# Performance work log

Measured on AMD Instinct MI355X. Metric: run time of the kernel, lower is better.

## Reference

```python
import jax, jax.numpy as jnp
import numpy as np

DILATIONS = (1, 2, 4, 8)
K = 3  # kernel_size
B, H, W, C = 16, 128, 128, 64
HID = 256
OUT = 64  # == C, so residual path is taken


def _depthwise(x, w, dilation):
    # x: [B,H,W,C], w: [K,K,1,C] (HWIO depthwise kernel)
    pad = dilation * (K // 2)
    return jax.lax.conv_general_dilated(
        x, w,
        window_strides=(1, 1),
        padding=[(pad, pad), (pad, pad)],
        rhs_dilation=(dilation, dilation),
        dimension_numbers=('NHWC', 'HWIO', 'NHWC'),
        feature_group_count=C,
    )


def setup_inputs() -> dict:
    key = jax.random.key(0)
    k_x, k_cw, k_w1, k_b1, k_w2, k_b2 = jax.random.split(key, 6)
    in_feat = C * (1 + len(DILATIONS))  # 320
    x = jax.random.normal(k_x, (B, H, W, C), jnp.float32)
    # depthwise kernels, one [K,K,1,C] per dilation, stacked
    conv_w = jax.random.normal(k_cw, (len(DILATIONS), K, K, 1, C), jnp.float32) * (1.0 / np.sqrt(K * K).astype(np.float32))
    W1 = jax.random.normal(k_w1, (in_feat, HID), jnp.float32) * np.float32(1.0 / np.sqrt(in_feat))
    b1 = jax.random.normal(k_b1, (HID,), jnp.float32) * 0.01
    W2 = jax.random.normal(k_w2, (HID, OUT), jnp.float32) * np.float32(1.0 / np.sqrt(HID))
    b2 = jax.random.normal(k_b2, (OUT,), jnp.float32) * 0.01
    return {"x": x, "conv_w": conv_w, "W1": W1, "b1": b1, "W2": W2, "b2": b2}


def reference(x, conv_w, W1, b1, W2, b2):
    # 1) Perception: multiscale depthwise dilated convs (same-padding per dilation)
    perceptions = [_depthwise(x, conv_w[i], d) for i, d in enumerate(DILATIONS)]
    upd_in = jnp.concatenate([x] + perceptions, axis=-1)  # [B,H,W,5C]
    # 2) Update MLP: Linear -> Dropout(eval: identity) -> GELU(exact erf) -> Linear
    h = jax.nn.gelu(upd_in @ W1 + b1, approximate=False)  # [B,H,W,HID]
    delta = h @ W2 + b2  # [B,H,W,OUT]
    # 3) out_channels == channels and (eval mode or fire_rate==1.0): plain residual
    return x + delta
```

## Files before the change

### kernel.cpp

```cpp
#include <hip/hip_runtime.h>
#include <hip/hip_fp16.h>
#include <cstdint>

#define B_   16
#define H_   128
#define W_   128
#define C_   64
#define HID_ 256
#define XELEMS (B_ * H_ * W_ * C_)

typedef _Float16 __attribute__((ext_vector_type(2))) half2v;
typedef _Float16 __attribute__((ext_vector_type(8))) half8v;
typedef __attribute__((ext_vector_type(4))) float f32x4;
typedef unsigned short ushort_t;

#define W1S_OFF 0
#define W2S_OFF 81920
#define CWH_OFF 98304
#define XH_OFF  100608
#define FEAT_OFF (XH_OFF + XELEMS)
#define FEAT_HALVES (4096ull * 16384ull)
#define WS_NEED_FULL (2ull * (FEAT_OFF + FEAT_HALVES))

__device__ __forceinline__ int hs(int row, int col) {
  return row * 256 + (((col >> 3) ^ (row & 7)) << 3) + (col & 7);
}

__device__ __forceinline__ float fast_gelu(float h) {
  float u = h * fmaf(h * h, 0.10293921f, 2.30211813f);
  float e = exp2f(-u);
  return h * __builtin_amdgcn_rcpf(1.0f + e);
}

__device__ __forceinline__ uint32_t fast_gelu_pk(float h0, float h1) {
  half2v h = __builtin_bit_cast(half2v, __builtin_amdgcn_cvt_pkrtz(h0, h1));
  const half2v c1 = {(_Float16)0.10293921f, (_Float16)0.10293921f};
  const half2v c0 = {(_Float16)2.30211813f, (_Float16)2.30211813f};
  half2v u = h * (c0 + h * h * c1);
  __half2 e = h2exp2(__hneg2(__builtin_bit_cast(__half2, u)));
  const __half2 one = __half2{(__half)1.0f, (__half)1.0f};
  __half2 s = h2rcp(__hadd2(one, e));
  __half2 g = __hmul2(__builtin_bit_cast(__half2, h), s);
  return __builtin_bit_cast(uint32_t, g);
}

__device__ __forceinline__ void stage16(const _Float16* g, ushort_t* l) {
  __builtin_amdgcn_global_load_lds(
      (const __attribute__((address_space(1))) void*)g,
      (__attribute__((address_space(3))) void*)l, 16, 0, 0);
}

__global__ void prep_kernel(const float* __restrict__ x,
                            const float* __restrict__ W1,
                            const float* __restrict__ W2,
                            const float* __restrict__ cw,
                            _Float16* __restrict__ wsb) {
  if (blockIdx.x < 393) {
    int t = blockIdx.x * 256 + threadIdx.x;
    if (t < 81920) {
      int j = t & 7, lane = (t >> 3) & 63, n16 = (t >> 9) & 15, ks = t >> 13;
      int k = ks * 32 + (lane >> 4) * 8 + j;
      int n = n16 * 16 + (lane & 15);
      wsb[W1S_OFF + t] = (_Float16)W1[k * 256 + n];
    } else if (t < 98304) {
      int t2 = t - 81920;
      int j = t2 & 7, lane = (t2 >> 3) & 63, n16 = (t2 >> 9) & 3, ks = t2 >> 11;
      int k = ks * 32 + (lane >> 4) * 8 + j;
      int n = n16 * 16 + (lane & 15);
      wsb[W2S_OFF + t2] = (_Float16)W2[k * 64 + n];
    } else if (t < 98304 + 2304) {
      int t3 = t - 98304;
      wsb[CWH_OFF + t3] = (_Float16)cw[t3];
    }
  } else {
    int i = ((blockIdx.x - 393) * 256 + threadIdx.x) * 8;
    const float4 a = *(const float4*)&x[i];
    const float4 b = *(const float4*)&x[i + 4];
    half8v o = {(_Float16)a.x, (_Float16)a.y, (_Float16)a.z, (_Float16)a.w,
                (_Float16)b.x, (_Float16)b.y, (_Float16)b.z, (_Float16)b.w};
    *(half8v*)&wsb[XH_OFF + i] = o;
  }
}

__global__ void conv_feat_kernel(const _Float16* __restrict__ xh,
                                 const _Float16* __restrict__ cwh,
                                 _Float16* __restrict__ feat) {
  const int tid   = threadIdx.x;
  const int tileX = blockIdx.x * 8;
  const int tileY = blockIdx.y * 8;
  const int batch = blockIdx.z >> 2;
  const int dd    = blockIdx.z & 3;
  const int dil   = 1 << dd;

  const _Float16* xhb = xh + (size_t)batch * (H_ * W_ * C_);
  _Float16* ft =
      feat + ((size_t)((batch * 16 + blockIdx.y) * 16 + blockIdx.x)) * 16384;

  const int quad = tid & 15;
  const int p0   = tid >> 4;
  const int ksq  = quad >> 3;
  const int c32  = (quad & 7) * 4;

  half2v w01[9], w23[9];
#pragma unroll
  for (int t = 0; t < 9; ++t) {
    uint2 wr = *(const uint2*)&cwh[(dd * 9 + t) * C_ + quad * 4];
    w01[t] = __builtin_bit_cast(half2v, wr.x);
    w23[t] = __builtin_bit_cast(half2v, wr.y);
  }

  uint2 v[4][9];
  const bool interior = (tileX >= 8) && (tileX <= W_ - 16) &&
                        (tileY >= 8) && (tileY <= H_ - 16);
  if (interior) {
#pragma unroll
    for (int i = 0; i < 4; ++i) {
      const int p  = i * 16 + p0;
      const int y0 = tileY + (p >> 3), x0 = tileX + (p & 7);
#pragma unroll
      for (int ky = 0; ky < 3; ++ky)
#pragma unroll
        for (int kx = 0; kx < 3; ++kx)
          v[i][ky * 3 + kx] = *(const uint2*)
              &xhb[((y0 + (ky - 1) * dil) * W_ + x0 + (kx - 1) * dil) * C_ +
                   quad * 4];
    }
  } else {
#pragma unroll
    for (int i = 0; i < 4; ++i) {
      const int p  = i * 16 + p0;
      const int y0 = tileY + (p >> 3), x0 = tileX + (p & 7);
#pragma unroll
      for (int ky = 0; ky < 3; ++ky)
#pragma unroll
        for (int kx = 0; kx < 3; ++kx) {
          const int yy = y0 + (ky - 1) * dil;
          const int xx = x0 + (kx - 1) * dil;
          uint2 vv = {0u, 0u};
          if ((unsigned)yy < (unsigned)H_ && (unsigned)xx < (unsigned)W_)
            vv = *(const uint2*)&xhb[(yy * W_ + xx) * C_ + quad * 4];
          v[i][ky * 3 + kx] = vv;
        }
    }
  }

#pragma unroll
  for (int i = 0; i < 4; ++i) {
    const int p = i * 16 + p0;
    half2v a01 = {0, 0}, a23 = {0, 0};
#pragma unroll
    for (int t = 0; t < 9; ++t) {
      a01 += __builtin_bit_cast(half2v, v[i][t].x) * w01[t];
      a23 += __builtin_bit_cast(half2v, v[i][t].y) * w23[t];
    }
    uint2 pk;
    pk.x = __builtin_bit_cast(uint32_t, a01);
    pk.y = __builtin_bit_cast(uint32_t, a23);
    *(uint2*)&ft[(dd * 2 + ksq) * 2048 + p * 32 + c32] = pk;
  }
}

__global__ __launch_bounds__(256, 4)
void mlp_kernel(const _Float16* __restrict__ xh,
                const _Float16* __restrict__ feat,
                const float* __restrict__ b1,
                const float* __restrict__ b2,
                const _Float16* __restrict__ w1s,
                const _Float16* __restrict__ w2s,
                float* __restrict__ out) {
  __shared__ __align__(16) ushort_t smem[64 * 256];

  const int tid   = threadIdx.x;
  const int tileX = blockIdx.x * 8;
  const int tileY = blockIdx.y * 8;
  const int batch = blockIdx.z;
  const _Float16* xhb = xh + (size_t)batch * (H_ * W_ * C_);
  const _Float16* ftb =
      feat + ((size_t)((batch * 16 + blockIdx.y) * 16 + blockIdx.x)) * 16384;

  const int lane = tid & 63;
  const int wv   = tid >> 6;
  const int lr   = lane & 15;
  const int lg   = lane >> 4;
  const int n0   = wv * 64;

  const half8v* w1v = (const half8v*)w1s;

  half8v xf[4][2];
#pragma unroll
  for (int pi = 0; pi < 4; ++pi) {
    const int p  = pi * 16 + lr;
    const int gp = (tileY + (p >> 3)) * W_ + tileX + (p & 7);
#pragma unroll
    for (int ks = 0; ks < 2; ++ks)
      xf[pi][ks] = *(const half8v*)&xhb[gp * C_ + ks * 32 + lg * 8];
  }

  {
    const _Float16* src0 = &ftb[(wv * 16 + lr) * 32 + lg * 8];
#pragma unroll
    for (int s = 0; s < 8; ++s)
      stage16(src0 + s * 2048, &smem[(s * 4 + wv) * 512]);
  }

  f32x4 acc[4][4];
#pragma unroll
  for (int hi = 0; hi < 4; ++hi)
#pragma unroll
    for (int pi = 0; pi < 4; ++pi) acc[hi][pi] = 0;

#pragma unroll
  for (int ks = 0; ks < 2; ++ks) {
    half8v wf[4];
#pragma unroll
    for (int hi = 0; hi < 4; ++hi)
      wf[hi] = w1v[(ks * 16 + wv * 4 + hi) * 64 + lane];
#pragma unroll
    for (int hi = 0; hi < 4; ++hi)
#pragma unroll
      for (int pi = 0; pi < 4; ++pi)
        acc[hi][pi] = __builtin_amdgcn_mfma_f32_16x16x32_f16(
            wf[hi], xf[pi][ks], acc[hi][pi], 0, 0, 0);
  }

  __syncthreads();

#define LOAD_W(WB, S)                                                         \
  _Pragma("unroll") for (int hi = 0; hi < 4; ++hi)                            \
      WB[hi] = w1v[((S) * 16 + wv * 4 + hi) * 64 + lane];
#define LOAD_F(FB, S)                                                         \
  _Pragma("unroll") for (int pi = 0; pi < 4; ++pi)                            \
      FB[pi] = *(const half8v*)&smem[(((S) - 2) * 4 + pi) * 512 + lane * 8];
#define MFMA16(WB, FB)                                                        \
  _Pragma("unroll") for (int hi = 0; hi < 4; ++hi)                            \
      _Pragma("unroll") for (int pi = 0; pi < 4; ++pi)                        \
      acc[hi][pi] = __builtin_amdgcn_mfma_f32_16x16x32_f16(                   \
          WB[hi], FB[pi], acc[hi][pi], 0, 0, 0);

  {
    half8v wfA[4], wfB[4], fA[4];
    LOAD_W(wfA, 2);
    LOAD_F(fA, 2); LOAD_W(wfB, 3); MFMA16(wfA, fA);
    LOAD_F(fA, 3); LOAD_W(wfA, 4); MFMA16(wfB, fA);
    LOAD_F(fA, 4); LOAD_W(wfB, 5); MFMA16(wfA, fA);
    LOAD_F(fA, 5); LOAD_W(wfA, 6); MFMA16(wfB, fA);
    LOAD_F(fA, 6); LOAD_W(wfB, 7); MFMA16(wfA, fA);
    LOAD_F(fA, 7); LOAD_W(wfA, 8); MFMA16(wfB, fA);
    LOAD_F(fA, 8); LOAD_W(wfB, 9); MFMA16(wfA, fA);
    LOAD_F(fA, 9);                 MFMA16(wfB, fA);
  }

  float4 bias1[4];
#pragma unroll
  for (int hi = 0; hi < 4; ++hi)
    bias1[hi] = *(const float4*)&b1[n0 + hi * 16 + lg * 4];

  __syncthreads();

#pragma unroll
  for (int hi = 0; hi < 4; ++hi) {
#pragma unroll
    for (int pi = 0; pi < 4; ++pi) {
      uint2 pk;
      pk.x = fast_gelu_pk(acc[hi][pi][0] + bias1[hi][0],
                          acc[hi][pi][1] + bias1[hi][1]);
      pk.y = fast_gelu_pk(acc[hi][pi][2] + bias1[hi][2],
                          acc[hi][pi][3] + bias1[hi][3]);
      *(uint2*)&smem[hs(pi * 16 + lr, n0 + hi * 16 + lg * 4)] = pk;
    }
  }
  __syncthreads();

  const int m0 = wv * 16;
  f32x4 acc2[4];
#pragma unroll
  for (int ni = 0; ni < 4; ++ni) acc2[ni] = 0;

  const half8v* w2v = (const half8v*)w2s;
#pragma unroll 2
  for (int ks = 0; ks < 8; ++ks) {
    half8v a2 = *(const half8v*)&smem[hs(m0 + lr, ks * 32 + lg * 8)];
#pragma unroll
    for (int ni = 0; ni < 4; ++ni) {
      half8v bfr = w2v[(ks * 4 + ni) * 64 + lane];
      acc2[ni] = __builtin_amdgcn_mfma_f32_16x16x32_f16(a2, bfr, acc2[ni],
                                                        0, 0, 0);
    }
  }

#pragma unroll
  for (int ni = 0; ni < 4; ++ni) {
    const int col  = ni * 16 + lr;
    const float bias = b2[col];
#pragma unroll
    for (int q = 0; q < 4; ++q) {
      const int row = m0 + lg * 4 + q;
      const int py = row >> 3, px = row & 7;
      const size_t idx =
          ((size_t)(batch * H_ + tileY + py) * W_ + (tileX + px)) * C_ + col;
      out[idx] = (float)xh[idx] + acc2[ni][q] + bias;
    }
  }
#undef LOAD_W
#undef LOAD_F
#undef MFMA16
}

template <bool BOUND>
__device__ __forceinline__ void conv_phase_f32(const float* __restrict__ xb,
                                               const _Float16* __restrict__ cwh,
                                               ushort_t* __restrict__ feat,
                                               int tid, int tileX, int tileY) {
  const int quad = tid & 15;
  const int p0   = tid >> 4;
#pragma unroll
  for (int dd = 0; dd < 4; ++dd) {
    const int dil = 1 << dd;
    half2v w01[9], w23[9];
#pragma unroll
    for (int t = 0; t < 9; ++t) {
      uint2 wr = *(const uint2*)&cwh[(dd * 9 + t) * C_ + quad * 4];
      w01[t] = __builtin_bit_cast(half2v, wr.x);
      w23[t] = __builtin_bit_cast(half2v, wr.y);
    }
#pragma unroll
    for (int i = 0; i < 4; ++i) {
      const int p  = i * 16 + p0;
      const int y0 = tileY + (p >> 3), x0 = tileX + (p & 7);
      half2v a01 = {0, 0}, a23 = {0, 0};
#pragma unroll
      for (int ky = 0; ky < 3; ++ky) {
        const int yy = y0 + (ky - 1) * dil;
        if (BOUND && (unsigned)yy >= (unsigned)H_) continue;
#pragma unroll
        for (int kx = 0; kx < 3; ++kx) {
          const int xx = x0 + (kx - 1) * dil;
          if (BOUND && (unsigned)xx >= (unsigned)W_) continue;
          const int t = ky * 3 + kx;
          const float4 xv = *(const float4*)&xb[(yy * W_ + xx) * C_ + quad * 4];
          half2v xl = {(_Float16)xv.x, (_Float16)xv.y};
          half2v xh2 = {(_Float16)xv.z, (_Float16)xv.w};
          a01 += xl * w01[t];
          a23 += xh2 * w23[t];
        }
      }
      uint2 pk;
      pk.x = __builtin_bit_cast(uint32_t, a01);
      pk.y = __builtin_bit_cast(uint32_t, a23);
      *(uint2*)&feat[hs(p, dd * 64 + quad * 4)] = pk;
    }
  }
}

__global__ __launch_bounds__(256, 4)
void nca_fused_fp32(const float* __restrict__ x,
                    const _Float16* __restrict__ cwh,
                    const float* __restrict__ b1,
                    const float* __restrict__ b2,
                    const _Float16* __restrict__ w1s,
                    const _Float16* __restrict__ w2s,
                    float* __restrict__ out) {
  __shared__ __align__(16) ushort_t smem[64 * 256];

  const int tid   = threadIdx.x;
  const int tileX = blockIdx.x * 8;
  const int tileY = blockIdx.y * 8;
  const int batch = blockIdx.z;
  const float* xb = x + (size_t)batch * (H_ * W_ * C_);

  const int lane = tid & 63;
  const int wv   = tid >> 6;
  const int lr   = lane & 15;
  const int lg   = lane >> 4;
  const int n0   = wv * 64;

  half8v xf[4][2];
#pragma unroll
  for (int pi = 0; pi < 4; ++pi) {
    const int p  = pi * 16 + lr;
    const int gp = (tileY + (p >> 3)) * W_ + tileX + (p & 7);
#pragma unroll
    for (int ks = 0; ks < 2; ++ks) {
      const float* bp = &xb[gp * C_ + ks * 32 + lg * 8];
      float4 u = *(const float4*)bp, v = *(const float4*)(bp + 4);
      half8v s = {(_Float16)u.x, (_Float16)u.y, (_Float16)u.z, (_Float16)u.w,
                  (_Float16)v.x, (_Float16)v.y, (_Float16)v.z, (_Float16)v.w};
      xf[pi][ks] = s;
    }
  }

  const bool interior = (tileX >= 8) && (tileX <= W_ - 16) &&
                        (tileY >= 8) && (tileY <= H_ - 16);
  if (interior)
    conv_phase_f32<false>(xb, cwh, smem, tid, tileX, tileY);
  else
    conv_phase_f32<true>(xb, cwh, smem, tid, tileX, tileY);
  __syncthreads();

  f32x4 acc[4][4];
#pragma unroll
  for (int hi = 0; hi < 4; ++hi)
#pragma unroll
    for (int pi = 0; pi < 4; ++pi) acc[hi][pi] = 0;

  const half8v* w1v = (const half8v*)w1s;
#pragma unroll
  for (int ks = 0; ks < 2; ++ks) {
    half8v wf[4];
#pragma unroll
    for (int hi = 0; hi < 4; ++hi)
      wf[hi] = w1v[(ks * 16 + wv * 4 + hi) * 64 + lane];
#pragma unroll
    for (int hi = 0; hi < 4; ++hi)
#pragma unroll
      for (int pi = 0; pi < 4; ++pi)
        acc[hi][pi] = __builtin_amdgcn_mfma_f32_16x16x32_f16(
            wf[hi], xf[pi][ks], acc[hi][pi], 0, 0, 0);
  }
  for (int ks = 2; ks < 10; ++ks) {
    half8v ff[4], wf[4];
#pragma unroll
    for (int pi = 0; pi < 4; ++pi)
      ff[pi] = *(const half8v*)&smem[hs(pi * 16 + lr, (ks - 2) * 32 + lg * 8)];
#pragma unroll
    for (int hi = 0; hi < 4; ++hi)
      wf[hi] = w1v[(ks * 16 + wv * 4 + hi) * 64 + lane];
#pragma unroll
    for (int hi = 0; hi < 4; ++hi)
#pragma unroll
      for (int pi = 0; pi < 4; ++pi)
        acc[hi][pi] = __builtin_amdgcn_mfma_f32_16x16x32_f16(
            wf[hi], ff[pi], acc[hi][pi], 0, 0, 0);
  }

  float4 bias1[4];
#pragma unroll
  for (int hi = 0; hi < 4; ++hi)
    bias1[hi] = *(const float4*)&b1[n0 + hi * 16 + lg * 4];

  __syncthreads();

#pragma unroll
  for (int hi = 0; hi < 4; ++hi) {
#pragma unroll
    for (int pi = 0; pi < 4; ++pi) {
      _Float16 g[4];
#pragma unroll
      for (int q = 0; q < 4; ++q)
        g[q] = (_Float16)fast_gelu(acc[hi][pi][q] + bias1[hi][q]);
      half2v g01 = {g[0], g[1]}, g23 = {g[2], g[3]};
      uint2 pk;
      pk.x = __builtin_bit_cast(uint32_t, g01);
      pk.y = __builtin_bit_cast(uint32_t, g23);
      *(uint2*)&smem[hs(pi * 16 + lr, n0 + hi * 16 + lg * 4)] = pk;
    }
  }
  __syncthreads();

  const int m0 = wv * 16;
  f32x4 acc2[4];
#pragma unroll
  for (int ni = 0; ni < 4; ++ni) acc2[ni] = 0;

  const half8v* w2v = (const half8v*)w2s;
  for (int ks = 0; ks < 8; ++ks) {
    half8v a2 = *(const half8v*)&smem[hs(m0 + lr, ks * 32 + lg * 8)];
#pragma unroll
    for (int ni = 0; ni < 4; ++ni) {
      half8v bfr = w2v[(ks * 4 + ni) * 64 + lane];
      acc2[ni] = __builtin_amdgcn_mfma_f32_16x16x32_f16(a2, bfr, acc2[ni],
                                                        0, 0, 0);
    }
  }

#pragma unroll
  for (int ni = 0; ni < 4; ++ni) {
    const int col  = ni * 16 + lr;
    const float bias = b2[col];
#pragma unroll
    for (int q = 0; q < 4; ++q) {
      const int row = m0 + lg * 4 + q;
      const int py = row >> 3, px = row & 7;
      const size_t idx =
          ((size_t)(batch * H_ + tileY + py) * W_ + (tileX + px)) * C_ + col;
      out[idx] = x[idx] + acc2[ni][q] + bias;
    }
  }
}

extern "C" void kernel_launch(void* const* d_in, const int* in_sizes, int n_in,
                              void* d_out, int out_size, void* d_ws,
                              size_t ws_size, hipStream_t stream) {
  const float* x  = (const float*)d_in[0];
  const float* cw = (const float*)d_in[1];
  const float* W1 = (const float*)d_in[2];
  const float* b1 = (const float*)d_in[3];
  const float* W2 = (const float*)d_in[4];
  const float* b2 = (const float*)d_in[5];
  float* out = (float*)d_out;

  _Float16* wsb  = (_Float16*)d_ws;
  _Float16* w1s  = wsb + W1S_OFF;
  _Float16* w2s  = wsb + W2S_OFF;
  _Float16* cwh  = wsb + CWH_OFF;
  _Float16* xh   = wsb + XH_OFF;
  _Float16* feat = wsb + FEAT_OFF;

  if (ws_size >= (size_t)WS_NEED_FULL) {
    prep_kernel<<<393 + XELEMS / 8 / 256, 256, 0, stream>>>(x, W1, W2, cw, wsb);
    dim3 cgrid(W_ / 8, H_ / 8, B_ * 4);
    conv_feat_kernel<<<cgrid, 256, 0, stream>>>(xh, cwh, feat);
    dim3 mgrid(W_ / 8, H_ / 8, B_);
    mlp_kernel<<<mgrid, 256, 0, stream>>>(xh, feat, b1, b2, w1s, w2s, out);
  } else {
    prep_kernel<<<393, 256, 0, stream>>>(x, W1, W2, cw, wsb);
    dim3 grid(W_ / 8, H_ / 8, B_);
    nca_fused_fp32<<<grid, 256, 0, stream>>>(x, cwh, b1, b2, w1s, w2s, out);
  }
}
```

Measured before the change: 190.8 us.

## Split depthwise conv per dilation with LDS-staged halo tiles

Replaces the single conv_feat kernel, which looped over all dilations by blockIdx.z, with separate templated kernels per dilation. For dilations 1, 2 and 4, interior tiles stage the haloed input tile into LDS via global_load_lds and compute taps from shared memory, removing repeated global reads of overlapping neighbours. Dilation 8 uses a kernel with 16-byte vector loads straight from global memory. The cost is four launches instead of one, a sync per block, and LDS use that may limit occupancy.

```diff
diff --git a/kernel.cpp b/kernel.cpp
--- a/kernel.cpp
+++ b/kernel.cpp
@@ -44,10 +44,14 @@
   return __builtin_bit_cast(uint32_t, g);
 }
 
-__device__ __forceinline__ void stage16(const _Float16* g, ushort_t* l) {
+__device__ __forceinline__ void stage16(const _Float16* g, const ushort_t* l) {
   __builtin_amdgcn_global_load_lds(
       (const __attribute__((address_space(1))) void*)g,
       (__attribute__((address_space(3))) void*)l, 16, 0, 0);
+}
+
+__device__ __forceinline__ half2v bch(uint32_t u) {
+  return __builtin_bit_cast(half2v, u);
 }
 
 __global__ void prep_kernel(const float* __restrict__ x,
@@ -82,20 +86,11 @@
   }
 }
 
-__global__ void conv_feat_kernel(const _Float16* __restrict__ xh,
-                                 const _Float16* __restrict__ cwh,
-                                 _Float16* __restrict__ feat) {
-  const int tid   = threadIdx.x;
-  const int tileX = blockIdx.x * 8;
-  const int tileY = blockIdx.y * 8;
-  const int batch = blockIdx.z >> 2;
-  const int dd    = blockIdx.z & 3;
-  const int dil   = 1 << dd;
-
-  const _Float16* xhb = xh + (size_t)batch * (H_ * W_ * C_);
-  _Float16* ft =
-      feat + ((size_t)((batch * 16 + blockIdx.y) * 16 + blockIdx.x)) * 16384;
-
+template <int DIL, int DDI>
+__device__ void conv_boundary(const _Float16* __restrict__ xhb,
+                              const _Float16* __restrict__ cwh,
+                              _Float16* __restrict__ ft,
+                              int tid, int tileX, int tileY) {
   const int quad = tid & 15;
   const int p0   = tid >> 4;
   const int ksq  = quad >> 3;
@@ -104,59 +99,174 @@
   half2v w01[9], w23[9];
 #pragma unroll
   for (int t = 0; t < 9; ++t) {
-    uint2 wr = *(const uint2*)&cwh[(dd * 9 + t) * C_ + quad * 4];
-    w01[t] = __builtin_bit_cast(half2v, wr.x);
-    w23[t] = __builtin_bit_cast(half2v, wr.y);
-  }
-
-  uint2 v[4][9];
-  const bool interior = (tileX >= 8) && (tileX <= W_ - 16) &&
-                        (tileY >= 8) && (tileY <= H_ - 16);
-  if (interior) {
-#pragma unroll
-    for (int i = 0; i < 4; ++i) {
-      const int p  = i * 16 + p0;
-      const int y0 = tileY + (p >> 3), x0 = tileX + (p & 7);
-#pragma unroll
-      for (int ky = 0; ky < 3; ++ky)
-#pragma unroll
-        for (int kx = 0; kx < 3; ++kx)
-          v[i][ky * 3 + kx] = *(const uint2*)
-              &xhb[((y0 + (ky - 1) * dil) * W_ + x0 + (kx - 1) * dil) * C_ +
-                   quad * 4];
-    }
-  } else {
-#pragma unroll
-    for (int i = 0; i < 4; ++i) {
-      const int p  = i * 16 + p0;
-      const int y0 = tileY + (p >> 3), x0 = tileX + (p & 7);
-#pragma unroll
-      for (int ky = 0; ky < 3; ++ky)
-#pragma unroll
-        for (int kx = 0; kx < 3; ++kx) {
-          const int yy = y0 + (ky - 1) * dil;
-          const int xx = x0 + (kx - 1) * dil;
-          uint2 vv = {0u, 0u};
-          if ((unsigned)yy < (unsigned)H_ && (unsigned)xx < (unsigned)W_)
-            vv = *(const uint2*)&xhb[(yy * W_ + xx) * C_ + quad * 4];
-          v[i][ky * 3 + kx] = vv;
-        }
-    }
-  }
-
+    uint2 wr = *(const uint2*)&cwh[(DDI * 9 + t) * C_ + quad * 4];
+    w01[t] = bch(wr.x);
+    w23[t] = bch(wr.y);
+  }
 #pragma unroll
   for (int i = 0; i < 4; ++i) {
-    const int p = i * 16 + p0;
+    const int p  = i * 16 + p0;
+    const int y0 = tileY + (p >> 3), x0 = tileX + (p & 7);
     half2v a01 = {0, 0}, a23 = {0, 0};
 #pragma unroll
-    for (int t = 0; t < 9; ++t) {
-      a01 += __builtin_bit_cast(half2v, v[i][t].x) * w01[t];
-      a23 += __builtin_bit_cast(half2v, v[i][t].y) * w23[t];
+    for (int ky = 0; ky < 3; ++ky) {
+      const int yy = y0 + (ky - 1) * DIL;
+#pragma unroll
+      for (int kx = 0; kx < 3; ++kx) {
+        const int xx = x0 + (kx - 1) * DIL;
+        uint2 vv = {0u, 0u};
+        if ((unsigned)yy < (unsigned)H_ && (unsigned)xx < (unsigned)W_)
+          vv = *(const uint2*)&xhb[(yy * W_ + xx) * C_ + quad * 4];
+        const int t = ky * 3 + kx;
+        a01 += bch(vv.x) * w01[t];
+        a23 += bch(vv.y) * w23[t];
+      }
     }
     uint2 pk;
     pk.x = __builtin_bit_cast(uint32_t, a01);
     pk.y = __builtin_bit_cast(uint32_t, a23);
-    *(uint2*)&ft[(dd * 2 + ksq) * 2048 + p * 32 + c32] = pk;
+    *(uint2*)&ft[(DDI * 2 + ksq) * 2048 + p * 32 + c32] = pk;
+  }
+}
+
+template <int DIL, int DDI>
+__global__ __launch_bounds__(256)
+void conv_lds_kernel(const _Float16* __restrict__ xh,
+                     const _Float16* __restrict__ cwh,
+                     _Float16* __restrict__ feat) {
+  constexpr int R = 8 + 2 * DIL;
+  __shared__ __align__(16) ushort_t lds[R * 1024];
+
+  const int tid   = threadIdx.x;
+  const int tileX = blockIdx.x * 8;
+  const int tileY = blockIdx.y * 8;
+  const int batch = blockIdx.z;
+  const _Float16* xhb = xh + (size_t)batch * (H_ * W_ * C_);
+  _Float16* ft =
+      feat + ((size_t)((batch * 16 + blockIdx.y) * 16 + blockIdx.x)) * 16384;
+
+  const bool interior = (tileX >= 8) && (tileX <= W_ - 16) &&
+                        (tileY >= 8) && (tileY <= H_ - 16);
+  if (!interior) {
+    conv_boundary<DIL, DDI>(xhb, cwh, ft, tid, tileX, tileY);
+    return;
+  }
+
+  const int lane = tid & 63;
+  const int wv   = tid >> 6;
+  const int quad = tid & 15;
+  const int p0   = tid >> 4;
+  const int ksq  = quad >> 3;
+  const int c32  = (quad & 7) * 4;
+
+  {
+    const int x0 = tileX - DIL, y0 = tileY - DIL;
+    for (int s = wv; s < 2 * R; s += 4) {
+      const int row = s >> 1, half = s & 1;
+      const _Float16* g = &xhb[((y0 + row) * W_ + x0 + half * 8 + (lane >> 3)) * C_ +
+                               (lane & 7) * 8];
+      stage16(g, &lds[row * 1024 + half * 512]);
+    }
+  }
+
+  half2v w01[9], w23[9];
+#pragma unroll
+  for (int t = 0; t < 9; ++t) {
+    uint2 wr = *(const uint2*)&cwh[(DDI * 9 + t) * C_ + quad * 4];
+    w01[t] = bch(wr.x);
+    w23[t] = bch(wr.y);
+  }
+
+  __syncthreads();
+
+#pragma unroll
+  for (int i = 0; i < 4; ++i) {
+    const int p  = i * 16 + p0;
+    const int py = p >> 3, px = p & 7;
+    uint2 tv[9];
+#pragma unroll
+    for (int ky = 0; ky < 3; ++ky)
+#pragma unroll
+      for (int kx = 0; kx < 3; ++kx)
+        tv[ky * 3 + kx] = *(const uint2*)
+            &lds[(py + ky * DIL) * 1024 + (px + kx * DIL) * 64 + quad * 4];
+    half2v a01 = {0, 0}, a23 = {0, 0};
+#pragma unroll
+    for (int t = 0; t < 9; ++t) {
+      a01 += bch(tv[t].x) * w01[t];
+      a23 += bch(tv[t].y) * w23[t];
+    }
+    uint2 pk;
+    pk.x = __builtin_bit_cast(uint32_t, a01);
+    pk.y = __builtin_bit_cast(uint32_t, a23);
+    *(uint2*)&ft[(DDI * 2 + ksq) * 2048 + p * 32 + c32] = pk;
+  }
+}
+
+__global__ __launch_bounds__(256)
+void conv_d8_kernel(const _Float16* __restrict__ xh,
+                    const _Float16* __restrict__ cwh,
+                    _Float16* __restrict__ feat) {
+  const int tid   = threadIdx.x;
+  const int tileX = blockIdx.x * 8;
+  const int tileY = blockIdx.y * 8;
+  const int batch = blockIdx.z;
+  const _Float16* xhb = xh + (size_t)batch * (H_ * W_ * C_);
+  _Float16* ft =
+      feat + ((size_t)((batch * 16 + blockIdx.y) * 16 + blockIdx.x)) * 16384;
+
+  const int c8 = tid & 7;
+  const int p0 = tid >> 3;
+  const int ksq = c8 >> 2;
+  const int cof = (c8 & 3) * 8;
+
+  uint4 wv4[9];
+#pragma unroll
+  for (int t = 0; t < 9; ++t)
+    wv4[t] = *(const uint4*)&cwh[(3 * 9 + t) * C_ + c8 * 8];
+
+  const bool interior = (tileX >= 8) && (tileX <= W_ - 16) &&
+                        (tileY >= 8) && (tileY <= H_ - 16);
+
+#pragma unroll
+  for (int i = 0; i < 2; ++i) {
+    const int p  = i * 32 + p0;
+    const int y0 = tileY + (p >> 3), x0 = tileX + (p & 7);
+    uint4 v[9];
+    if (interior) {
+#pragma unroll
+      for (int ky = 0; ky < 3; ++ky)
+#pragma unroll
+        for (int kx = 0; kx < 3; ++kx)
+          v[ky * 3 + kx] = *(const uint4*)
+              &xhb[((y0 + (ky - 1) * 8) * W_ + x0 + (kx - 1) * 8) * C_ + c8 * 8];
+    } else {
+#pragma unroll
+      for (int ky = 0; ky < 3; ++ky)
+#pragma unroll
+        for (int kx = 0; kx < 3; ++kx) {
+          const int yy = y0 + (ky - 1) * 8;
+          const int xx = x0 + (kx - 1) * 8;
+          uint4 vv = {0u, 0u, 0u, 0u};
+          if ((unsigned)yy < (unsigned)H_ && (unsigned)xx < (unsigned)W_)
+            vv = *(const uint4*)&xhb[(yy * W_ + xx) * C_ + c8 * 8];
+          v[ky * 3 + kx] = vv;
+        }
+    }
+    half2v a0 = {0, 0}, a1 = {0, 0}, a2 = {0, 0}, a3 = {0, 0};
+#pragma unroll
+    for (int t = 0; t < 9; ++t) {
+      a0 += bch(v[t].x) * bch(wv4[t].x);
+      a1 += bch(v[t].y) * bch(wv4[t].y);
+      a2 += bch(v[t].z) * bch(wv4[t].z);
+      a3 += bch(v[t].w) * bch(wv4[t].w);
+    }
+    uint4 pk;
+    pk.x = __builtin_bit_cast(uint32_t, a0);
+    pk.y = __builtin_bit_cast(uint32_t, a1);
+    pk.z = __builtin_bit_cast(uint32_t, a2);
+    pk.w = __builtin_bit_cast(uint32_t, a3);
+    *(uint4*)&ft[(3 * 2 + ksq) * 2048 + p * 32 + cof] = pk;
   }
 }
 
@@ -320,8 +430,8 @@
 #pragma unroll
     for (int t = 0; t < 9; ++t) {
       uint2 wr = *(const uint2*)&cwh[(dd * 9 + t) * C_ + quad * 4];
-      w01[t] = __builtin_bit_cast(half2v, wr.x);
-      w23[t] = __builtin_bit_cast(half2v, wr.y);
+      w01[t] = bch(wr.x);
+      w23[t] = bch(wr.y);
     }
 #pragma unroll
     for (int i = 0; i < 4; ++i) {
@@ -508,10 +618,12 @@
 
   if (ws_size >= (size_t)WS_NEED_FULL) {
     prep_kernel<<<393 + XELEMS / 8 / 256, 256, 0, stream>>>(x, W1, W2, cw, wsb);
-    dim3 cgrid(W_ / 8, H_ / 8, B_ * 4);
-    conv_feat_kernel<<<cgrid, 256, 0, stream>>>(xh, cwh, feat);
-    dim3 mgrid(W_ / 8, H_ / 8, B_);
-    mlp_kernel<<<mgrid, 256, 0, stream>>>(xh, feat, b1, b2, w1s, w2s, out);
+    dim3 g16(W_ / 8, H_ / 8, B_);
+    conv_lds_kernel<1, 0><<<g16, 256, 0, stream>>>(xh, cwh, feat);
+    conv_lds_kernel<2, 1><<<g16, 256, 0, stream>>>(xh, cwh, feat);
+    conv_lds_kernel<4, 2><<<g16, 256, 0, stream>>>(xh, cwh, feat);
+    conv_d8_kernel<<<g16, 256, 0, stream>>>(xh, cwh, feat);
+    mlp_kernel<<<g16, 256, 0, stream>>>(xh, feat, b1, b2, w1s, w2s, out);
   } else {
     prep_kernel<<<393, 256, 0, stream>>>(x, W1, W2, cw, wsb);
     dim3 grid(W_ / 8, H_ / 8, B_);
```

Result: slower. 198.4 us (+4.0%).
